# Kernel optimization log

Hardware: AMD Instinct MI355X
Metric: run time of the kernel (lower is better)

Reference implementation:

```python
import jax, jax.numpy as jnp
import numpy as np

B = 8192; N_LEAF = 34; N_SUB = 11; D0 = 32; ES = 64; EA = 128; H = 4
ETH = slice(0, 8); IP = slice(8, 19); TCP = slice(19, 34)
TCPF = slice(0, 8); IPF = slice(8, 11)


def setup_inputs() -> dict:
    key = jax.random.key(0)
    ks = jax.random.split(key, 32)
    w = lambda i, s: jax.random.normal(ks[i], s, dtype=jnp.float32) * 0.05
    return {
        "leaf_feats": jax.random.normal(ks[0], (B, N_LEAF, D0), dtype=jnp.float32),
        "sub_feats": jax.random.normal(ks[1], (B, N_SUB, D0), dtype=jnp.float32),
        "sub_align_W": w(2, (N_SUB, D0, ES)), "sub_align_b": w(3, (N_SUB, ES)),
        "leaf_align_W": w(4, (N_LEAF, D0, EA)), "leaf_align_b": w(5, (N_LEAF, EA)),
        "parent_align_W": w(6, (2, ES, EA)), "parent_align_b": w(7, (2, EA)),
        "sA_cls": w(8, (2, ES)), "sA_Wqkv": w(9, (2, 3 * ES, ES)), "sA_bqkv": w(10, (2, 3 * ES)),
        "sA_Wo": w(11, (2, ES, ES)), "sA_bo": w(12, (2, ES)),
        "sA_lng": jnp.ones((2, ES), jnp.float32), "sA_lnb": jnp.zeros((2, ES), jnp.float32),
        "sA_W1": w(13, (2, ES, 4 * ES)), "sA_b1": w(14, (2, 4 * ES)),
        "sA_W2": w(15, (2, 4 * ES, ES)), "sA_b2": w(16, (2, ES)),
        "pA_cls": w(17, (4, EA)), "pA_Wqkv": w(18, (4, 3 * EA, EA)), "pA_bqkv": w(19, (4, 3 * EA)),
        "pA_Wo": w(20, (4, EA, EA)), "pA_bo": w(21, (4, EA)),
        "pA_lng": jnp.ones((4, EA), jnp.float32), "pA_lnb": jnp.zeros((4, EA), jnp.float32),
        "pA_W1": w(22, (4, EA, 4 * EA)), "pA_b1": w(23, (4, 4 * EA)),
        "pA_W2": w(24, (4, 4 * EA, EA)), "pA_b2": w(25, (4, EA)),
        "clf_W": w(26, (EA, 2)), "clf_b": w(27, (2,)),
    }


def _ln(t, g, b):
    m = jnp.mean(t, -1, keepdims=True)
    v = jnp.var(t, -1, keepdims=True)
    return (t - m) / jnp.sqrt(v + 1e-5) * g + b


def _agg(x, cls, Wqkv, bqkv, Wo, bo, lng, lnb, W1, b1, W2, b2):
    # AttentionAggregator: prepend CLS, MHA, shared LayerNorm twice, FFN; return CLS output.
    Bx, _, E = x.shape
    d = E // H
    xc = jnp.concatenate([jnp.broadcast_to(cls, (Bx, 1, E)), x], axis=1)  # [B,S,E]
    S = xc.shape[1]
    qkv = xc @ Wqkv.T + bqkv                      # torch MHA in_proj layout [3E,E]
    q, k, v = jnp.split(qkv, 3, axis=-1)
    sh = lambda t: t.reshape(Bx, S, H, d).transpose(0, 2, 1, 3)
    q, k, v = sh(q), sh(k), sh(v)
    a = jax.nn.softmax(jnp.einsum('bhqd,bhkd->bhqk', q, k) * (1.0 / np.sqrt(d)), axis=-1)
    o = jnp.einsum('bhqk,bhkd->bhqd', a, v).transpose(0, 2, 1, 3).reshape(Bx, S, E)
    o = o @ Wo.T + bo
    h = _ln(xc + o, lng, lnb)
    f = jax.nn.gelu(h @ W1 + b1, approximate=False) @ W2 + b2
    h = _ln(h + f, lng, lnb)
    return h[:, 0]


def reference(leaf_feats, sub_feats, sub_align_W, sub_align_b, leaf_align_W, leaf_align_b,
              parent_align_W, parent_align_b,
              sA_cls, sA_Wqkv, sA_bqkv, sA_Wo, sA_bo, sA_lng, sA_lnb, sA_W1, sA_b1, sA_W2, sA_b2,
              pA_cls, pA_Wqkv, pA_bqkv, pA_Wo, pA_bo, pA_lng, pA_lnb, pA_W1, pA_b1, pA_W2, pA_b2,
              clf_W, clf_b):
    sA = lambda i: (sA_cls[i], sA_Wqkv[i], sA_bqkv[i], sA_Wo[i], sA_bo[i], sA_lng[i], sA_lnb[i],
                    sA_W1[i], sA_b1[i], sA_W2[i], sA_b2[i])
    pA = lambda i: (pA_cls[i], pA_Wqkv[i], pA_bqkv[i], pA_Wo[i], pA_bo[i], pA_lng[i], pA_lnb[i],
                    pA_W1[i], pA_b1[i], pA_W2[i], pA_b2[i])
    # subfield align (per-subfield Linear, batched) + aggregate
    sub_al = jnp.einsum('bsd,sde->bse', sub_feats, sub_align_W) + sub_align_b  # [B,11,64]
    tcpf = _agg(sub_al[:, TCPF], *sA(0))   # tcp.flags -> [B,64]
    ipf = _agg(sub_al[:, IPF], *sA(1))     # ip.flags  -> [B,64]
    # per-field aligners to aligned_dim=128
    leaf_al = jnp.einsum('bfd,fde->bfe', leaf_feats, leaf_align_W) + leaf_align_b  # [B,34,128]
    parent_al = jnp.stack([tcpf @ parent_align_W[0] + parent_align_b[0],
                           ipf @ parent_align_W[1] + parent_align_b[1]], axis=1)   # [B,2,128]
    eth_vec = _agg(leaf_al[:, ETH], *pA(0))
    ip_vec = _agg(jnp.concatenate([leaf_al[:, IP], parent_al[:, 1:2]], axis=1), *pA(1))
    tcp_vec = _agg(jnp.concatenate([leaf_al[:, TCP], parent_al[:, 0:1]], axis=1), *pA(2))
    pkt = _agg(jnp.stack([eth_vec, ip_vec, tcp_vec], axis=1), *pA(3))
    return pkt @ clf_W + clf_b
```

## Files before the change

### kernel.cpp

```cpp
#include <hip/hip_runtime.h>
#include <math.h>

#define NT 256
#define G 4


enum {
  I_LEAF = 0, I_SUB, I_SAW, I_SAB, I_LAW, I_LAB, I_PAW, I_PAB,
  I_SCLS, I_SWQKV, I_SBQKV, I_SWO, I_SBO, I_SLNG, I_SLNB, I_SW1, I_SB1, I_SW2, I_SB2,
  I_PCLS, I_PWQKV, I_PBQKV, I_PWO, I_PBO, I_PLNG, I_PLNB, I_PW1, I_PB1, I_PW2, I_PB2,
  I_CLFW, I_CLFB
};

struct P {
  const float* in[32];
  float* parent_al;
  float* vecs;
  float* out;
};

__device__ float g_usb[6][520];

__device__ __forceinline__ void LD8(const float* p, float* o) {
  float4 a = ((const float4*)p)[0], b = ((const float4*)p)[1];
  o[0] = a.x; o[1] = a.y; o[2] = a.z; o[3] = a.w;
  o[4] = b.x; o[5] = b.y; o[6] = b.z; o[7] = b.w;
}
__device__ __forceinline__ void fma8(float& acc, const float* x, const float* w) {
#pragma unroll
  for (int i = 0; i < 8; ++i) acc += x[i] * w[i];
}
__device__ __forceinline__ float gelu(float v) {
  return 0.5f * v * (1.0f + erff(v * 0.70710678118654752f));
}

template <int E>
__device__ void ln_rows(float* buf, const float* __restrict__ gg, const float* __restrict__ bb) {
  const int w = threadIdx.x >> 6, lane = threadIdx.x & 63;
  for (int g = w; g < G; g += 4) {
    float* row = buf + g * E;
    float s = 0.f, s2 = 0.f;
    for (int e = lane; e < E; e += 64) { float x = row[e]; s += x; s2 += x * x; }
#pragma unroll
    for (int off = 1; off < 64; off <<= 1) {
      s += __shfl_xor(s, off, 64);
      s2 += __shfl_xor(s2, off, 64);
    }
    float m = s / (float)E;
    float inv = 1.0f / sqrtf(s2 / (float)E - m * m + 1e-5f);
    for (int e = lane; e < E; e += 64) row[e] = (row[e] - m) * inv * gg[e] + bb[e];
  }
}

__global__ __launch_bounds__(NT) void k_setup(P p) {
  const int a = blockIdx.x;
  const int tid = threadIdx.x;
  __shared__ float clsb[128];
  __shared__ float qb[128];
  int E;
  const float *Wq, *bq, *cls;
  if (a < 2) {
    E = 64;
    Wq = p.in[I_SWQKV] + (size_t)a * 192 * 64;
    bq = p.in[I_SBQKV] + a * 192;
    cls = p.in[I_SCLS] + a * 64;
  } else {
    E = 128;
    int i = a - 2;
    Wq = p.in[I_PWQKV] + (size_t)i * 384 * 128;
    bq = p.in[I_PBQKV] + i * 384;
    cls = p.in[I_PCLS] + i * 128;
  }
  const int D = E / 4;
  const float scale = (E == 64) ? 0.25f : 0.17677669529663687f;
  if (tid < E) clsb[tid] = cls[tid];
  __syncthreads();
  if (tid < E) {
    float acc = bq[tid];
    const float* w = Wq + (size_t)tid * E;
    for (int k = 0; k < E; k += 8) {
      float wv[8];
      LD8(w + k, wv);
#pragma unroll
      for (int ii = 0; ii < 8; ++ii) acc += clsb[k + ii] * wv[ii];
    }
    qb[tid] = acc;
  }
  __syncthreads();
  if (tid < E) {
    for (int h = 0; h < 4; ++h) {
      float acc = 0.f;
      for (int d = 0; d < D; ++d)
        acc += Wq[(size_t)(E + h * D + d) * E + tid] * qb[h * D + d];
      g_usb[a][h * E + tid] = acc * scale;
    }
  }
  if (tid < 4) {
    float acc = 0.f;
    for (int d = 0; d < D; ++d) acc += qb[tid * D + d] * bq[E + tid * D + d];
    g_usb[a][4 * E + tid] = acc * scale;
  }
}

template <int E, int T, int XP>
__device__ void agg_run(const float* X, const float* clsb,
                        const float* uL, const float* sbL,
                        const float* __restrict__ Wv, const float* __restrict__ bv,
                        const float* __restrict__ Wo, const float* __restrict__ bo,
                        const float* __restrict__ lng, const float* __restrict__ lnb,
                        const float* __restrict__ W1, const float* __restrict__ b1,
                        const float* __restrict__ W2, const float* __restrict__ b2,
                        float* att, float* xbar, float* ob, float* hb, float* mid,
                        float* partial) {
  const int tid = threadIdx.x;
  constexpr int S = T + 1, KS = NT / E, KCH = E / KS;
  constexpr int M1 = (4 * E) / NT, KCH2 = (4 * E) / KS;

  for (int i = tid; i < G * 4 * S; i += NT) {
    int s = i % S, hh = (i / S) % 4, g = i / (4 * S);
    const float* u = uL + hh * XP;
    const float* x = (s == 0) ? clsb : (X + (size_t)((s - 1) * G + g) * XP);
    float acc = sbL[hh];
    for (int k = 0; k < E; k += 8) {
      float xv[8], uv[8];
      LD8(x + k, xv);
      LD8(u + k, uv);
      fma8(acc, xv, uv);
    }
    att[(g * 4 + hh) * S + s] = acc;
  }
  __syncthreads();
  for (int i = tid; i < G * 4; i += NT) {
    float* a = att + i * S;
    float mx = a[0];
    for (int s = 1; s < S; ++s) mx = fmaxf(mx, a[s]);
    float sum = 0.f;
    for (int s = 0; s < S; ++s) { float e = expf(a[s] - mx); a[s] = e; sum += e; }
    float inv = 1.0f / sum;
    for (int s = 0; s < S; ++s) a[s] *= inv;
  }
  __syncthreads();
  constexpr int NI = (G * 4 * E) / NT;
  float xacc[NI];
#pragma unroll
  for (int n = 0; n < NI; ++n) {
    int i = tid + n * NT;
    int k = i % E, hh = (i / E) % 4, g = i / (4 * E);
    const float* a = att + (g * 4 + hh) * S;
    float acc = a[0] * clsb[k];
    for (int s = 1; s < S; ++s) acc += a[s] * X[(size_t)((s - 1) * G + g) * XP + k];
    xacc[n] = acc;
  }
  __syncthreads();
#pragma unroll
  for (int n = 0; n < NI; ++n) xbar[tid + n * NT] = xacc[n];
  __syncthreads();
  {
    const int e = tid % E, ks = tid / E, hh = e / (E / 4);
    const float* w = Wv + (size_t)e * E + ks * KCH;
    float acc[G];
#pragma unroll
    for (int g = 0; g < G; ++g) acc[g] = 0.f;
    for (int kc = 0; kc < KCH; kc += 8) {
      float wv[8];
      LD8(w + kc, wv);
#pragma unroll
      for (int g = 0; g < G; ++g) {
        float xv[8];
        LD8(xbar + (g * 4 + hh) * E + ks * KCH + kc, xv);
        fma8(acc[g], xv, wv);
      }
    }
#pragma unroll
    for (int g = 0; g < G; ++g) partial[(ks * G + g) * E + e] = acc[g];
  }
  __syncthreads();
  for (int i = tid; i < G * E; i += NT) {
    int e = i % E, g = i / E;
    float v = bv[e];
#pragma unroll
    for (int ks = 0; ks < KS; ++ks) v += partial[(ks * G + g) * E + e];
    ob[g * E + e] = v;
  }
  __syncthreads();
  {
    const int e = tid % E, ks = tid / E;
    const float* w = Wo + (size_t)e * E + ks * KCH;
    float acc[G];
#pragma unroll
    for (int g = 0; g < G; ++g) acc[g] = 0.f;
    for (int kc = 0; kc < KCH; kc += 8) {
      float wv[8];
      LD8(w + kc, wv);
#pragma unroll
      for (int g = 0; g < G; ++g) {
        float xv[8];
        LD8(ob + g * E + ks * KCH + kc, xv);
        fma8(acc[g], xv, wv);
      }
    }
#pragma unroll
    for (int g = 0; g < G; ++g) partial[(ks * G + g) * E + e] = acc[g];
  }
  __syncthreads();
  for (int i = tid; i < G * E; i += NT) {
    int e = i % E, g = i / E;
    float v = bo[e] + clsb[e];
#pragma unroll
    for (int ks = 0; ks < KS; ++ks) v += partial[(ks * G + g) * E + e];
    hb[g * E + e] = v;
  }
  __syncthreads();
  ln_rows<E>(hb, lng, lnb);
  __syncthreads();
  {
    float acc[M1][G];
#pragma unroll
    for (int r = 0; r < M1; ++r)
#pragma unroll
      for (int g = 0; g < G; ++g) acc[r][g] = 0.f;
    for (int j = 0; j < E; j += 8) {
      float wv[M1][8];
#pragma unroll
      for (int ii = 0; ii < 8; ++ii) {
        if constexpr (M1 == 2) {
          float2 w2 = *(const float2*)(W1 + (size_t)(j + ii) * 4 * E + 2 * tid);
          wv[0][ii] = w2.x;
          wv[1][ii] = w2.y;
        } else {
          wv[0][ii] = W1[(size_t)(j + ii) * 4 * E + tid];
        }
      }
#pragma unroll
      for (int g = 0; g < G; ++g) {
        float xv[8];
        LD8(hb + g * E + j, xv);
#pragma unroll
        for (int r = 0; r < M1; ++r) fma8(acc[r][g], xv, wv[r]);
      }
    }
#pragma unroll
    for (int r = 0; r < M1; ++r) {
      int m = tid * M1 + r;
      float bias = b1[m];
#pragma unroll
      for (int g = 0; g < G; ++g) mid[g * 4 * E + m] = gelu(acc[r][g] + bias);
    }
  }
  __syncthreads();
  {
    const int e = tid % E, ks = tid / E, m0 = ks * KCH2;
    float acc[G];
#pragma unroll
    for (int g = 0; g < G; ++g) acc[g] = 0.f;
    for (int mc = 0; mc < KCH2; mc += 8) {
      float wv[8];
#pragma unroll
      for (int ii = 0; ii < 8; ++ii) wv[ii] = W2[(size_t)(m0 + mc + ii) * E + e];
#pragma unroll
      for (int g = 0; g < G; ++g) {
        float xv[8];
        LD8(mid + g * 4 * E + m0 + mc, xv);
        fma8(acc[g], xv, wv);
      }
    }
#pragma unroll
    for (int g = 0; g < G; ++g) partial[(ks * G + g) * E + e] = acc[g];
  }
  __syncthreads();
  for (int i = tid; i < G * E; i += NT) {
    int e = i % E, g = i / E;
    float v = b2[e] + hb[g * E + e];
#pragma unroll
    for (int ks = 0; ks < KS; ++ks) v += partial[(ks * G + g) * E + e];
    ob[g * E + e] = v;
  }
  __syncthreads();
  ln_rows<E>(ob, lng, lnb);
  __syncthreads();
}

__global__ __launch_bounds__(NT, 4) void k_sub(P p) {
  constexpr int XP = 68;
  __shared__ __align__(16) float X1[8 * G * XP];
  __shared__ __align__(16) float X2[3 * G * XP];
  __shared__ __align__(16) float clsb[64];
  __shared__ __align__(16) float uL[4 * XP];
  __shared__ __align__(16) float sbL[4];
  __shared__ __align__(16) float att[G * 4 * 9];
  __shared__ __align__(16) float xbar[G * 4 * 64];
  __shared__ __align__(16) float ob[G * 64];
  __shared__ __align__(16) float hb[G * 64];
  __shared__ __align__(16) float mid[G * 256];
  __shared__ __align__(16) float partial[4 * G * 64];
  __shared__ __align__(16) float vec1[G * 64];
  const int tid = threadIdx.x, b0 = blockIdx.x * G;

  const float* subf = p.in[I_SUB];
  const float* saW = p.in[I_SAW];
  const float* sab = p.in[I_SAB];
  for (int i = tid; i < 11 * 64; i += NT) {
    int f = i / 64, e = i % 64;
    float bias = sab[f * 64 + e];
    float acc[G];
#pragma unroll
    for (int g = 0; g < G; ++g) acc[g] = bias;
    for (int d = 0; d < 32; d += 8) {
      float wv[8];
#pragma unroll
      for (int ii = 0; ii < 8; ++ii) wv[ii] = saW[(size_t)(f * 32 + d + ii) * 64 + e];
#pragma unroll
      for (int g = 0; g < G; ++g) {
        float xv[8];
        LD8(subf + (size_t)(b0 + g) * 352 + f * 32 + d, xv);
        fma8(acc[g], xv, wv);
      }
    }
#pragma unroll
    for (int g = 0; g < G; ++g) {
      if (f < 8) X1[(f * G + g) * XP + e] = acc[g];
      else       X2[((f - 8) * G + g) * XP + e] = acc[g];
    }
  }
  for (int i = tid; i < 4 * 64; i += NT) uL[(i >> 6) * XP + (i & 63)] = g_usb[0][i];
  if (tid < 4) sbL[tid] = g_usb[0][256 + tid];
  if (tid < 64) clsb[tid] = p.in[I_SCLS][tid];
  __syncthreads();

  agg_run<64, 8, XP>(X1, clsb, uL, sbL,
                     p.in[I_SWQKV] + 2 * 64 * 64, p.in[I_SBQKV] + 128,
                     p.in[I_SWO], p.in[I_SBO], p.in[I_SLNG], p.in[I_SLNB],
                     p.in[I_SW1], p.in[I_SB1], p.in[I_SW2], p.in[I_SB2],
                     att, xbar, ob, hb, mid, partial);
  for (int i = tid; i < G * 64; i += NT) vec1[i] = ob[i];

  for (int i = tid; i < 4 * 64; i += NT) uL[(i >> 6) * XP + (i & 63)] = g_usb[1][i];
  if (tid < 4) sbL[tid] = g_usb[1][256 + tid];
  if (tid < 64) clsb[tid] = p.in[I_SCLS][64 + tid];
  __syncthreads();

  agg_run<64, 3, XP>(X2, clsb, uL, sbL,
                     p.in[I_SWQKV] + 192 * 64 + 2 * 64 * 64, p.in[I_SBQKV] + 192 + 128,
                     p.in[I_SWO] + 64 * 64, p.in[I_SBO] + 64,
                     p.in[I_SLNG] + 64, p.in[I_SLNB] + 64,
                     p.in[I_SW1] + 64 * 256, p.in[I_SB1] + 256,
                     p.in[I_SW2] + 256 * 64, p.in[I_SB2] + 64,
                     att, xbar, ob, hb, mid, partial);

  {
    const int pi = tid >> 7, e = tid & 127;
    const float* paW = p.in[I_PAW];
    float bias = p.in[I_PAB][pi * 128 + e];
    float acc[G];
#pragma unroll
    for (int g = 0; g < G; ++g) acc[g] = bias;
    const float* src = pi ? ob : vec1;
    for (int j = 0; j < 64; j += 8) {
      float wv[8];
#pragma unroll
      for (int ii = 0; ii < 8; ++ii) wv[ii] = paW[(size_t)(pi * 64 + j + ii) * 128 + e];
#pragma unroll
      for (int g = 0; g < G; ++g) {
        float xv[8];
        LD8(src + g * 64 + j, xv);
        fma8(acc[g], xv, wv);
      }
    }
#pragma unroll
    for (int g = 0; g < G; ++g)
      p.parent_al[(size_t)(b0 + g) * 256 + pi * 128 + e] = acc[g];
  }
}

#define PXP 132

template <int T, int F, int F0, int PAR, int AI>
__device__ void parent_body(const P& p, int b0, float* arena, float* clsb,
                            float* uL, float* sbL, float* att) {
  const int tid = threadIdx.x;
  float* X = arena;
  const float* leaf = p.in[I_LEAF];
  const float* laW = p.in[I_LAW];
  const float* lab = p.in[I_LAB];
  for (int i = tid; i < F * 128; i += NT) {
    int f = i / 128, e = i % 128;
    float bias = lab[(F0 + f) * 128 + e];
    float acc[G];
#pragma unroll
    for (int g = 0; g < G; ++g) acc[g] = bias;
    for (int d = 0; d < 32; d += 8) {
      float wv[8];
#pragma unroll
      for (int ii = 0; ii < 8; ++ii)
        wv[ii] = laW[(size_t)((F0 + f) * 32 + d + ii) * 128 + e];
#pragma unroll
      for (int g = 0; g < G; ++g) {
        float xv[8];
        LD8(leaf + (size_t)(b0 + g) * 1088 + (F0 + f) * 32 + d, xv);
        fma8(acc[g], xv, wv);
      }
    }
#pragma unroll
    for (int g = 0; g < G; ++g) X[(f * G + g) * PXP + e] = acc[g];
  }
  if constexpr (PAR >= 0) {
    for (int i = tid; i < G * 128; i += NT) {
      int g = i / 128, e = i % 128;
      X[((T - 1) * G + g) * PXP + e] = p.parent_al[(size_t)(b0 + g) * 256 + PAR * 128 + e];
    }
  }
  for (int i = tid; i < 4 * 128; i += NT) uL[(i >> 7) * PXP + (i & 127)] = g_usb[2 + AI][i];
  if (tid < 4) sbL[tid] = g_usb[2 + AI][512 + tid];
  if (tid < 128) clsb[tid] = p.in[I_PCLS][AI * 128 + tid];
  __syncthreads();

  float* xbar = arena;
  float* partial = arena + 2048;
  float* ob = arena + 3072;
  float* hb = arena + 3584;
  float* mid = arena + 4096;
  agg_run<128, T, PXP>(X, clsb, uL, sbL,
                       p.in[I_PWQKV] + (size_t)AI * 384 * 128 + 2 * 128 * 128,
                       p.in[I_PBQKV] + AI * 384 + 256,
                       p.in[I_PWO] + (size_t)AI * 128 * 128, p.in[I_PBO] + AI * 128,
                       p.in[I_PLNG] + AI * 128, p.in[I_PLNB] + AI * 128,
                       p.in[I_PW1] + (size_t)AI * 128 * 512, p.in[I_PB1] + AI * 512,
                       p.in[I_PW2] + (size_t)AI * 512 * 128, p.in[I_PB2] + AI * 128,
                       att, xbar, ob, hb, mid, partial);
  for (int i = tid; i < G * 128; i += NT) {
    int e = i % 128, g = i / 128;
    p.vecs[(size_t)(b0 + g) * 384 + AI * 128 + e] = ob[g * 128 + e];
  }
}

__global__ __launch_bounds__(NT, 4) void k_parent(P p) {
  __shared__ __align__(16) float arena[16 * G * PXP];
  __shared__ __align__(16) float clsb[128];
  __shared__ __align__(16) float uL[4 * PXP];
  __shared__ __align__(16) float sbL[4];
  __shared__ __align__(16) float att[G * 4 * 17];
  const int b0 = blockIdx.x * G;
  if (blockIdx.y == 0)
    parent_body<8, 8, 0, -1, 0>(p, b0, arena, clsb, uL, sbL, att);
  else if (blockIdx.y == 1)
    parent_body<12, 11, 8, 1, 1>(p, b0, arena, clsb, uL, sbL, att);
  else
    parent_body<16, 15, 19, 0, 2>(p, b0, arena, clsb, uL, sbL, att);
}

__global__ __launch_bounds__(NT, 4) void k_pkt(P p) {
  __shared__ __align__(16) float arena[6144];
  __shared__ __align__(16) float clsb[128];
  __shared__ __align__(16) float uL[4 * PXP];
  __shared__ __align__(16) float sbL[4];
  __shared__ __align__(16) float att[G * 4 * 4];
  const int tid = threadIdx.x, b0 = blockIdx.x * G;
  float* X = arena;

  for (int i = tid; i < 3 * G * 128; i += NT) {
    int e = i % 128, g = (i / 128) % G, t = i / (G * 128);
    X[(t * G + g) * PXP + e] = p.vecs[(size_t)(b0 + g) * 384 + t * 128 + e];
  }
  for (int i = tid; i < 4 * 128; i += NT) uL[(i >> 7) * PXP + (i & 127)] = g_usb[5][i];
  if (tid < 4) sbL[tid] = g_usb[5][512 + tid];
  if (tid < 128) clsb[tid] = p.in[I_PCLS][3 * 128 + tid];
  __syncthreads();

  float* xbar = arena;
  float* partial = arena + 2048;
  float* ob = arena + 3072;
  float* hb = arena + 3584;
  float* mid = arena + 4096;
  agg_run<128, 3, PXP>(X, clsb, uL, sbL,
                       p.in[I_PWQKV] + (size_t)3 * 384 * 128 + 2 * 128 * 128,
                       p.in[I_PBQKV] + 3 * 384 + 256,
                       p.in[I_PWO] + (size_t)3 * 128 * 128, p.in[I_PBO] + 3 * 128,
                       p.in[I_PLNG] + 3 * 128, p.in[I_PLNB] + 3 * 128,
                       p.in[I_PW1] + (size_t)3 * 128 * 512, p.in[I_PB1] + 3 * 512,
                       p.in[I_PW2] + (size_t)3 * 512 * 128, p.in[I_PB2] + 3 * 128,
                       att, xbar, ob, hb, mid, partial);

  if (tid < G * 2) {
    int g = tid >> 1, c = tid & 1;
    const float* cw = p.in[I_CLFW];
    float acc = p.in[I_CLFB][c];
    for (int j = 0; j < 128; ++j) acc += ob[g * 128 + j] * cw[j * 2 + c];
    p.out[(size_t)(b0 + g) * 2 + c] = acc;
  }
}

extern "C" void kernel_launch(void* const* d_in, const int* in_sizes, int n_in,
                              void* d_out, int out_size, void* d_ws, size_t ws_size,
                              hipStream_t stream) {
  P p;
  for (int i = 0; i < 32; ++i) p.in[i] = (const float*)d_in[i];
  const int B = in_sizes[0] / (34 * 32);
  float* ws = (float*)d_ws;
  p.parent_al = ws;
  p.vecs = ws + (size_t)B * 256;
  p.out = (float*)d_out;

  k_setup<<<dim3(6), dim3(NT), 0, stream>>>(p);
  k_sub<<<dim3(B / G), dim3(NT), 0, stream>>>(p);
  k_parent<<<dim3(B / G, 3), dim3(NT), 0, stream>>>(p);
  k_pkt<<<dim3(B / G), dim3(NT), 0, stream>>>(p);
}
```

Before: 1.050 ms.

## Pre-transpose weight matrices so each thread reads contiguous vectorized rows

Adds a transpose kernel that writes the aligner, FFN W1 and FFN W2 weights into global buffers laid out so each output channel's reduction dimension is contiguous. The matmul loops then use 16-byte vector loads along a row instead of strided scalar loads across rows. Shared-memory activation buffers are also reordered from token-major to batch-major. The thread-to-row mapping now makes adjacent lanes read addresses a whole row apart, which can reduce coalescing. The weights are re-transposed by an extra launch on every call.

```diff
diff --git a/kernel.cpp b/kernel.cpp
--- a/kernel.cpp
+++ b/kernel.cpp
@@ -1,8 +1,8 @@
 #include <hip/hip_runtime.h>
 #include <math.h>
 
+#define G 4
 #define NT 256
-#define G 4
 
 
 enum {
@@ -20,6 +20,14 @@
 };
 
 __device__ float g_usb[6][520];
+
+__device__ __align__(16) float g_paWT[2 * 128 * 64];
+__device__ __align__(16) float g_laWT[34 * 128 * 32];
+__device__ __align__(16) float g_saWT[11 * 64 * 32];
+__device__ __align__(16) float g_sW1T[2 * 256 * 64];
+__device__ __align__(16) float g_sW2T[2 * 64 * 256];
+__device__ __align__(16) float g_pW1T[4 * 512 * 128];
+__device__ __align__(16) float g_pW2T[4 * 128 * 512];
 
 __device__ __forceinline__ void LD8(const float* p, float* o) {
   float4 a = ((const float4*)p)[0], b = ((const float4*)p)[1];
@@ -49,6 +57,46 @@
     float m = s / (float)E;
     float inv = 1.0f / sqrtf(s2 / (float)E - m * m + 1e-5f);
     for (int e = lane; e < E; e += 64) row[e] = (row[e] - m) * inv * gg[e] + bb[e];
+  }
+}
+
+__global__ __launch_bounds__(NT) void k_tr(P p) {
+  const int i0 = blockIdx.x * NT + threadIdx.x;
+  const int n = gridDim.x * NT;
+  const float* paW = p.in[I_PAW];
+  const float* laW = p.in[I_LAW];
+  const float* saW = p.in[I_SAW];
+  const float* sW1 = p.in[I_SW1];
+  const float* sW2 = p.in[I_SW2];
+  const float* pW1 = p.in[I_PW1];
+  const float* pW2 = p.in[I_PW2];
+  for (int idx = i0; idx < 2 * 128 * 64; idx += n) {
+    int pi = idx / 8192, r = idx % 8192, e = r / 64, j = r % 64;
+    g_paWT[idx] = paW[(size_t)(pi * 64 + j) * 128 + e];
+  }
+  for (int idx = i0; idx < 34 * 128 * 32; idx += n) {
+    int f = idx / 4096, r = idx % 4096, e = r / 32, d = r % 32;
+    g_laWT[idx] = laW[(size_t)(f * 32 + d) * 128 + e];
+  }
+  for (int idx = i0; idx < 11 * 64 * 32; idx += n) {
+    int f = idx / 2048, r = idx % 2048, e = r / 32, d = r % 32;
+    g_saWT[idx] = saW[(size_t)(f * 32 + d) * 64 + e];
+  }
+  for (int idx = i0; idx < 2 * 256 * 64; idx += n) {
+    int a = idx / 16384, r = idx % 16384, m = r / 64, j = r % 64;
+    g_sW1T[idx] = sW1[(size_t)(a * 64 + j) * 256 + m];
+  }
+  for (int idx = i0; idx < 2 * 64 * 256; idx += n) {
+    int a = idx / 16384, r = idx % 16384, e = r / 256, m = r % 256;
+    g_sW2T[idx] = sW2[(size_t)(a * 256 + m) * 64 + e];
+  }
+  for (int idx = i0; idx < 4 * 512 * 128; idx += n) {
+    int a = idx / 65536, r = idx % 65536, m = r / 128, j = r % 128;
+    g_pW1T[idx] = pW1[(size_t)(a * 128 + j) * 512 + m];
+  }
+  for (int idx = i0; idx < 4 * 128 * 512; idx += n) {
+    int a = idx / 65536, r = idx % 65536, e = r / 512, m = r % 512;
+    g_pW2T[idx] = pW2[(size_t)(a * 512 + m) * 128 + e];
   }
 }
 
@@ -108,8 +156,8 @@
                         const float* __restrict__ Wv, const float* __restrict__ bv,
                         const float* __restrict__ Wo, const float* __restrict__ bo,
                         const float* __restrict__ lng, const float* __restrict__ lnb,
-                        const float* __restrict__ W1, const float* __restrict__ b1,
-                        const float* __restrict__ W2, const float* __restrict__ b2,
+                        const float* __restrict__ W1T, const float* __restrict__ b1,
+                        const float* __restrict__ W2T, const float* __restrict__ b2,
                         float* att, float* xbar, float* ob, float* hb, float* mid,
                         float* partial) {
   const int tid = threadIdx.x;
@@ -119,7 +167,7 @@
   for (int i = tid; i < G * 4 * S; i += NT) {
     int s = i % S, hh = (i / S) % 4, g = i / (4 * S);
     const float* u = uL + hh * XP;
-    const float* x = (s == 0) ? clsb : (X + (size_t)((s - 1) * G + g) * XP);
+    const float* x = (s == 0) ? clsb : (X + (size_t)(g * T + s - 1) * XP);
     float acc = sbL[hh];
     for (int k = 0; k < E; k += 8) {
       float xv[8], uv[8];
@@ -148,7 +196,7 @@
     int k = i % E, hh = (i / E) % 4, g = i / (4 * E);
     const float* a = att + (g * 4 + hh) * S;
     float acc = a[0] * clsb[k];
-    for (int s = 1; s < S; ++s) acc += a[s] * X[(size_t)((s - 1) * G + g) * XP + k];
+    for (int s = 1; s < S; ++s) acc += a[s] * X[(size_t)(g * T + s - 1) * XP + k];
     xacc[n] = acc;
   }
   __syncthreads();
@@ -222,15 +270,7 @@
     for (int j = 0; j < E; j += 8) {
       float wv[M1][8];
 #pragma unroll
-      for (int ii = 0; ii < 8; ++ii) {
-        if constexpr (M1 == 2) {
-          float2 w2 = *(const float2*)(W1 + (size_t)(j + ii) * 4 * E + 2 * tid);
-          wv[0][ii] = w2.x;
-          wv[1][ii] = w2.y;
-        } else {
-          wv[0][ii] = W1[(size_t)(j + ii) * 4 * E + tid];
-        }
-      }
+      for (int r = 0; r < M1; ++r) LD8(W1T + (size_t)(tid * M1 + r) * E + j, wv[r]);
 #pragma unroll
       for (int g = 0; g < G; ++g) {
         float xv[8];
@@ -250,13 +290,13 @@
   __syncthreads();
   {
     const int e = tid % E, ks = tid / E, m0 = ks * KCH2;
+    const float* w = W2T + (size_t)e * (4 * E) + m0;
     float acc[G];
 #pragma unroll
     for (int g = 0; g < G; ++g) acc[g] = 0.f;
     for (int mc = 0; mc < KCH2; mc += 8) {
       float wv[8];
-#pragma unroll
-      for (int ii = 0; ii < 8; ++ii) wv[ii] = W2[(size_t)(m0 + mc + ii) * E + e];
+      LD8(w + mc, wv);
 #pragma unroll
       for (int g = 0; g < G; ++g) {
         float xv[8];
@@ -282,8 +322,8 @@
 
 __global__ __launch_bounds__(NT, 4) void k_sub(P p) {
   constexpr int XP = 68;
-  __shared__ __align__(16) float X1[8 * G * XP];
-  __shared__ __align__(16) float X2[3 * G * XP];
+  __shared__ __align__(16) float X1[G * 8 * XP];
+  __shared__ __align__(16) float X2[G * 3 * XP];
   __shared__ __align__(16) float clsb[64];
   __shared__ __align__(16) float uL[4 * XP];
   __shared__ __align__(16) float sbL[4];
@@ -297,18 +337,17 @@
   const int tid = threadIdx.x, b0 = blockIdx.x * G;
 
   const float* subf = p.in[I_SUB];
-  const float* saW = p.in[I_SAW];
   const float* sab = p.in[I_SAB];
   for (int i = tid; i < 11 * 64; i += NT) {
     int f = i / 64, e = i % 64;
     float bias = sab[f * 64 + e];
+    const float* wt = g_saWT + (size_t)i * 32;
     float acc[G];
 #pragma unroll
     for (int g = 0; g < G; ++g) acc[g] = bias;
     for (int d = 0; d < 32; d += 8) {
       float wv[8];
-#pragma unroll
-      for (int ii = 0; ii < 8; ++ii) wv[ii] = saW[(size_t)(f * 32 + d + ii) * 64 + e];
+      LD8(wt + d, wv);
 #pragma unroll
       for (int g = 0; g < G; ++g) {
         float xv[8];
@@ -318,8 +357,8 @@
     }
 #pragma unroll
     for (int g = 0; g < G; ++g) {
-      if (f < 8) X1[(f * G + g) * XP + e] = acc[g];
-      else       X2[((f - 8) * G + g) * XP + e] = acc[g];
+      if (f < 8) X1[(g * 8 + f) * XP + e] = acc[g];
+      else       X2[(g * 3 + f - 8) * XP + e] = acc[g];
     }
   }
   for (int i = tid; i < 4 * 64; i += NT) uL[(i >> 6) * XP + (i & 63)] = g_usb[0][i];
@@ -330,7 +369,7 @@
   agg_run<64, 8, XP>(X1, clsb, uL, sbL,
                      p.in[I_SWQKV] + 2 * 64 * 64, p.in[I_SBQKV] + 128,
                      p.in[I_SWO], p.in[I_SBO], p.in[I_SLNG], p.in[I_SLNB],
-                     p.in[I_SW1], p.in[I_SB1], p.in[I_SW2], p.in[I_SB2],
+                     g_sW1T, p.in[I_SB1], g_sW2T, p.in[I_SB2],
                      att, xbar, ob, hb, mid, partial);
   for (int i = tid; i < G * 64; i += NT) vec1[i] = ob[i];
 
@@ -343,22 +382,21 @@
                      p.in[I_SWQKV] + 192 * 64 + 2 * 64 * 64, p.in[I_SBQKV] + 192 + 128,
                      p.in[I_SWO] + 64 * 64, p.in[I_SBO] + 64,
                      p.in[I_SLNG] + 64, p.in[I_SLNB] + 64,
-                     p.in[I_SW1] + 64 * 256, p.in[I_SB1] + 256,
-                     p.in[I_SW2] + 256 * 64, p.in[I_SB2] + 64,
+                     g_sW1T + 256 * 64, p.in[I_SB1] + 256,
+                     g_sW2T + 64 * 256, p.in[I_SB2] + 64,
                      att, xbar, ob, hb, mid, partial);
 
   {
     const int pi = tid >> 7, e = tid & 127;
-    const float* paW = p.in[I_PAW];
     float bias = p.in[I_PAB][pi * 128 + e];
+    const float* wt = g_paWT + (size_t)(pi * 128 + e) * 64;
     float acc[G];
 #pragma unroll
     for (int g = 0; g < G; ++g) acc[g] = bias;
     const float* src = pi ? ob : vec1;
     for (int j = 0; j < 64; j += 8) {
       float wv[8];
-#pragma unroll
-      for (int ii = 0; ii < 8; ++ii) wv[ii] = paW[(size_t)(pi * 64 + j + ii) * 128 + e];
+      LD8(wt + j, wv);
 #pragma unroll
       for (int g = 0; g < G; ++g) {
         float xv[8];
@@ -380,19 +418,17 @@
   const int tid = threadIdx.x;
   float* X = arena;
   const float* leaf = p.in[I_LEAF];
-  const float* laW = p.in[I_LAW];
   const float* lab = p.in[I_LAB];
   for (int i = tid; i < F * 128; i += NT) {
     int f = i / 128, e = i % 128;
     float bias = lab[(F0 + f) * 128 + e];
+    const float* wt = g_laWT + ((size_t)(F0 + f) * 128 + e) * 32;
     float acc[G];
 #pragma unroll
     for (int g = 0; g < G; ++g) acc[g] = bias;
     for (int d = 0; d < 32; d += 8) {
       float wv[8];
-#pragma unroll
-      for (int ii = 0; ii < 8; ++ii)
-        wv[ii] = laW[(size_t)((F0 + f) * 32 + d + ii) * 128 + e];
+      LD8(wt + d, wv);
 #pragma unroll
       for (int g = 0; g < G; ++g) {
         float xv[8];
@@ -401,12 +437,12 @@
       }
     }
 #pragma unroll
-    for (int g = 0; g < G; ++g) X[(f * G + g) * PXP + e] = acc[g];
+    for (int g = 0; g < G; ++g) X[(g * T + f) * PXP + e] = acc[g];
   }
   if constexpr (PAR >= 0) {
     for (int i = tid; i < G * 128; i += NT) {
       int g = i / 128, e = i % 128;
-      X[((T - 1) * G + g) * PXP + e] = p.parent_al[(size_t)(b0 + g) * 256 + PAR * 128 + e];
+      X[(g * T + T - 1) * PXP + e] = p.parent_al[(size_t)(b0 + g) * 256 + PAR * 128 + e];
     }
   }
   for (int i = tid; i < 4 * 128; i += NT) uL[(i >> 7) * PXP + (i & 127)] = g_usb[2 + AI][i];
@@ -424,8 +460,8 @@
                        p.in[I_PBQKV] + AI * 384 + 256,
                        p.in[I_PWO] + (size_t)AI * 128 * 128, p.in[I_PBO] + AI * 128,
                        p.in[I_PLNG] + AI * 128, p.in[I_PLNB] + AI * 128,
-                       p.in[I_PW1] + (size_t)AI * 128 * 512, p.in[I_PB1] + AI * 512,
-                       p.in[I_PW2] + (size_t)AI * 512 * 128, p.in[I_PB2] + AI * 128,
+                       g_pW1T + (size_t)AI * 512 * 128, p.in[I_PB1] + AI * 512,
+                       g_pW2T + (size_t)AI * 128 * 512, p.in[I_PB2] + AI * 128,
                        att, xbar, ob, hb, mid, partial);
   for (int i = tid; i < G * 128; i += NT) {
     int e = i % 128, g = i / 128;
@@ -434,7 +470,7 @@
 }
 
 __global__ __launch_bounds__(NT, 4) void k_parent(P p) {
-  __shared__ __align__(16) float arena[16 * G * PXP];
+  __shared__ __align__(16) float arena[G * 16 * PXP];
   __shared__ __align__(16) float clsb[128];
   __shared__ __align__(16) float uL[4 * PXP];
   __shared__ __align__(16) float sbL[4];
@@ -459,7 +495,7 @@
 
   for (int i = tid; i < 3 * G * 128; i += NT) {
     int e = i % 128, g = (i / 128) % G, t = i / (G * 128);
-    X[(t * G + g) * PXP + e] = p.vecs[(size_t)(b0 + g) * 384 + t * 128 + e];
+    X[(g * 3 + t) * PXP + e] = p.vecs[(size_t)(b0 + g) * 384 + t * 128 + e];
   }
   for (int i = tid; i < 4 * 128; i += NT) uL[(i >> 7) * PXP + (i & 127)] = g_usb[5][i];
   if (tid < 4) sbL[tid] = g_usb[5][512 + tid];
@@ -476,8 +512,8 @@
                        p.in[I_PBQKV] + 3 * 384 + 256,
                        p.in[I_PWO] + (size_t)3 * 128 * 128, p.in[I_PBO] + 3 * 128,
                        p.in[I_PLNG] + 3 * 128, p.in[I_PLNB] + 3 * 128,
-                       p.in[I_PW1] + (size_t)3 * 128 * 512, p.in[I_PB1] + 3 * 512,
-                       p.in[I_PW2] + (size_t)3 * 512 * 128, p.in[I_PB2] + 3 * 128,
+                       g_pW1T + (size_t)3 * 512 * 128, p.in[I_PB1] + 3 * 512,
+                       g_pW2T + (size_t)3 * 128 * 512, p.in[I_PB2] + 3 * 128,
                        att, xbar, ob, hb, mid, partial);
 
   if (tid < G * 2) {
@@ -500,6 +536,7 @@
   p.vecs = ws + (size_t)B * 256;
   p.out = (float*)d_out;
 
+  k_tr<<<dim3(512), dim3(NT), 0, stream>>>(p);
   k_setup<<<dim3(6), dim3(NT), 0, stream>>>(p);
   k_sub<<<dim3(B / G), dim3(NT), 0, stream>>>(p);
   k_parent<<<dim3(B / G, 3), dim3(NT), 0, stream>>>(p);
```

Result: slower. 1.388 ms (+32.2%).
